# Kernel tuning notes

Measured on AMD Instinct MI355X. Metric: run time of the kernel, lower is better.

The kernel has to match this reference:

```python
import jax, jax.numpy as jnp
import numpy as np

B, N, DIM, H, DH = 4, 1024, 512, 8, 64
INNER = H * DH
LN_EPS = 1e-5


def layernorm(x, g, b):
    m = x.mean(-1, keepdims=True)
    v = jnp.var(x, axis=-1, keepdims=True)
    return (x - m) / jnp.sqrt(v + LN_EPS) * g + b


def setup_inputs() -> dict:
    key = jax.random.key(0)
    ks = jax.random.split(key, 8)
    return {
        "q": jax.random.normal(ks[0], (B, N, DIM), jnp.float32),
        "k": jax.random.normal(ks[1], (B, N, DIM), jnp.float32),
        "v": jax.random.normal(ks[2], (B, N, DIM), jnp.float32),
        "ln_g": jnp.ones((DIM,), jnp.float32),
        "ln_b": jnp.zeros((DIM,), jnp.float32),
        "W_in": jax.random.normal(ks[3], (INNER, DIM), jnp.float32) * 0.02,
        "W_out": jax.random.normal(ks[4], (DIM, INNER), jnp.float32) * 0.02,
        "b_out": jnp.zeros((DIM,), jnp.float32),
        "wp_W1": jax.random.normal(ks[5], (DH, 2 * DH), jnp.float32) * 0.05,
        "wp_b1": jnp.zeros((DH,), jnp.float32),
        "wp_ln_g": jnp.ones((DH,), jnp.float32),
        "wp_ln_b": jnp.zeros((DH,), jnp.float32),
        "wp_W2": jax.random.normal(ks[6], (3, DH), jnp.float32) * 0.05,
        "wp_b2": jnp.zeros((3,), jnp.float32),
    }


def reference(q, k, v, ln_g, ln_b, W_in, W_out, b_out,
              wp_W1, wp_b1, wp_ln_g, wp_ln_b, wp_W2, wp_b2):
    b, n, _ = q.shape

    def proj(t):  # [b, n, dim] -> [h, b, n, d]
        y = layernorm(t, ln_g, ln_b) @ W_in.T
        return y.reshape(b, n, H, DH).transpose(2, 0, 1, 3)

    f_q, f_k, f_v = proj(q), proj(k), proj(v)

    # cosine similarity component: [h, b, n, m]
    dots = jnp.einsum('hbnd,hbmd->hbnm', f_q, f_k)
    qn = jnp.linalg.norm(f_q, axis=-1)  # [h, b, n]
    kn = jnp.linalg.norm(f_k, axis=-1)  # [h, b, m]
    cosine_sim = dots / (qn[..., :, None] * kn[..., None, :])

    # centered covariance component
    q_c = f_q - f_q.mean(-1, keepdims=True)
    k_c = f_k - f_k.mean(-1, keepdims=True)
    cov_component = jnp.einsum('hbnd,hbmd->hbnm', q_c, k_c) / DH

    # variance-product component (outer product of per-row variances, unbiased like torch.var)
    q_var = jnp.var(f_q, axis=-1, ddof=1)  # [h, b, n]
    k_var = jnp.var(f_k, axis=-1, ddof=1)  # [h, b, m]
    var_component = (q_var[..., :, None] * k_var[..., None, :]) / DH

    # dynamic per-head mixing weights
    q_global = f_q.mean(axis=(1, 2))  # [h, d]
    k_global = f_k.mean(axis=(1, 2))  # [h, d]
    feats = jnp.concatenate([q_global, k_global], axis=-1)  # [h, 2d]
    hdn = jax.nn.relu(layernorm(feats @ wp_W1.T + wp_b1, wp_ln_g, wp_ln_b))
    weights = jax.nn.softmax(hdn @ wp_W2.T + wp_b2, axis=-1)  # [h, 3]
    w = weights[:, :, None, None, None]  # [h, 3, 1, 1, 1]

    mixed = w[:, 0] * cosine_sim + w[:, 1] * cov_component + w[:, 2] * var_component
    out = jnp.einsum('hbnm,hbmd->hbnd', mixed, f_v)
    out = out.transpose(1, 2, 0, 3).reshape(b, n, INNER)  # 'h b n d -> b n (h d)'
    return out @ W_out.T + b_out
```

## Files before the change

### kernel.cpp

```cpp
#include <hip/hip_runtime.h>
#include <hip/hip_bf16.h>

#define LN_EPS 1e-5f
typedef __attribute__((ext_vector_type(8))) short short8v;
typedef __attribute__((ext_vector_type(4))) short short4v;
typedef __attribute__((ext_vector_type(4))) float f32x4;
typedef __hip_bfloat16 bf16;

__device__ inline float wred_sum(float v) {
#pragma unroll
  for (int off = 1; off < 64; off <<= 1) v += __shfl_xor(v, off, 64);
  return v;
}
__device__ inline float b2f(short s) {
  return __uint_as_float(((unsigned)(unsigned short)s) << 16);
}
__device__ inline short f2bs(float x) {
  union { bf16 h; short s; } u; u.h = __float2bfloat16(x); return u.s;
}
__device__ inline float rbf(float x) {
  return __bfloat162float(__float2bfloat16(x));
}

__global__ __launch_bounds__(256) void lncvt_kernel(
    const float* __restrict__ q, const float* __restrict__ k,
    const float* __restrict__ v,
    const float* __restrict__ g, const float* __restrict__ bln,
    const float* __restrict__ Wi, const float* __restrict__ Wo,
    bf16* __restrict__ abf, bf16* __restrict__ Wib, bf16* __restrict__ Wob) {
  int bid = blockIdx.x, tid = threadIdx.x;
  if (bid < 3072) {
    int wave = tid >> 6, lane = tid & 63;
    int grow = bid * 4 + wave;
    int tensor = grow >> 12, row = grow & 4095;
    const float* src = tensor == 0 ? q : (tensor == 1 ? k : v);
    const float4* p = (const float4*)(src + (size_t)row * 512 + lane * 8);
    float4 a = p[0], b = p[1];
    float s  = a.x + a.y + a.z + a.w + b.x + b.y + b.z + b.w;
    float ss = a.x*a.x + a.y*a.y + a.z*a.z + a.w*a.w
             + b.x*b.x + b.y*b.y + b.z*b.z + b.w*b.w;
    s = wred_sum(s);
    ss = wred_sum(ss);
    float m = s * (1.f / 512.f);
    float r = rsqrtf(ss * (1.f / 512.f) - m * m + LN_EPS);
    float4 g0 = *(const float4*)(g + lane * 8);
    float4 g1 = *(const float4*)(g + lane * 8 + 4);
    float4 b0 = *(const float4*)(bln + lane * 8);
    float4 b1 = *(const float4*)(bln + lane * 8 + 4);
    short8v t;
    t[0] = f2bs((a.x - m) * r * g0.x + b0.x);
    t[1] = f2bs((a.y - m) * r * g0.y + b0.y);
    t[2] = f2bs((a.z - m) * r * g0.z + b0.z);
    t[3] = f2bs((a.w - m) * r * g0.w + b0.w);
    t[4] = f2bs((b.x - m) * r * g1.x + b1.x);
    t[5] = f2bs((b.y - m) * r * g1.y + b1.y);
    t[6] = f2bs((b.z - m) * r * g1.z + b1.z);
    t[7] = f2bs((b.w - m) * r * g1.w + b1.w);
    *(short8v*)(abf + (size_t)grow * 512 + lane * 8) = t;
  } else {
    int e0 = ((bid - 3072) * 256 + tid) * 8;
    float4 a = *(const float4*)(Wi + e0);
    float4 b = *(const float4*)(Wi + e0 + 4);
    short8v t;
    t[0] = f2bs(a.x); t[1] = f2bs(a.y); t[2] = f2bs(a.z); t[3] = f2bs(a.w);
    t[4] = f2bs(b.x); t[5] = f2bs(b.y); t[6] = f2bs(b.z); t[7] = f2bs(b.w);
    *(short8v*)(Wib + e0) = t;
    a = *(const float4*)(Wo + e0);
    b = *(const float4*)(Wo + e0 + 4);
    t[0] = f2bs(a.x); t[1] = f2bs(a.y); t[2] = f2bs(a.z); t[3] = f2bs(a.w);
    t[4] = f2bs(b.x); t[5] = f2bs(b.y); t[6] = f2bs(b.z); t[7] = f2bs(b.w);
    *(short8v*)(Wob + e0) = t;
  }
}

__global__ __launch_bounds__(256) void proj_kernel(
    const bf16* __restrict__ Asrc, const bf16* __restrict__ Wb,
    bf16* __restrict__ f_q, bf16* __restrict__ fkt, bf16* __restrict__ fkh,
    bf16* __restrict__ fvt,
    float* __restrict__ rn, float* __restrict__ mn, float* __restrict__ vr,
    float* __restrict__ gp) {
  __shared__ __attribute__((aligned(16))) bf16 As[64 * 64];
  __shared__ __attribute__((aligned(16))) bf16 Bs[128 * 64];
  __shared__ float gpbuf[4][128];
  int tid = threadIdx.x;
  int bj = blockIdx.x, bi = blockIdx.y;
  int row0 = bi * 64;
  int wv = tid >> 6, l = tid & 63, fr = l & 15, lq = l >> 4;
  f32x4 acc[8];
#pragma unroll
  for (int j = 0; j < 8; ++j)
#pragma unroll
    for (int e = 0; e < 4; ++e) acc[j][e] = 0.f;

  int swz = (fr & 7) << 4;

  for (int ks = 0; ks < 512; ks += 64) {
#pragma unroll
    for (int c = 0; c < 2; ++c) {
      int off = wv * 2048 + c * 1024 + l * 16;
      int ar = off >> 7;
      int sc = (off & 127) ^ ((ar & 7) << 4);
      const char* gsrc = (const char*)(Asrc + (size_t)(row0 + ar) * 512 + ks) + sc;
      __builtin_amdgcn_global_load_lds(gsrc, (char*)As + wv * 2048 + c * 1024, 16, 0, 0);
    }
#pragma unroll
    for (int c = 0; c < 4; ++c) {
      int off = wv * 4096 + c * 1024 + l * 16;
      int br = off >> 7;
      int sc = (off & 127) ^ ((br & 7) << 4);
      const char* gsrc = (const char*)(Wb + (size_t)(bj * 128 + br) * 512 + ks) + sc;
      __builtin_amdgcn_global_load_lds(gsrc, (char*)Bs + wv * 4096 + c * 1024, 16, 0, 0);
    }
    __syncthreads();
#pragma unroll
    for (int kk = 0; kk < 64; kk += 32) {
      int csw = (kk * 2 + lq * 16) ^ swz;
      short8v af = *(const short8v*)&As[(wv * 16 + fr) * 64 + (csw >> 1)];
#pragma unroll
      for (int j = 0; j < 8; ++j) {
        short8v bv = *(const short8v*)&Bs[(j * 16 + fr) * 64 + (csw >> 1)];
        acc[j] = __builtin_amdgcn_mfma_f32_16x16x32_bf16(af, bv, acc[j], 0, 0, 0);
      }
    }
    __syncthreads();
  }

  int tensor = bi >> 6, rb = bi & 63;
  int b = rb >> 4, n0 = (rb & 15) * 64;
  int nbase = n0 + wv * 16 + lq * 4;
  if (tensor == 2) {
#pragma unroll
    for (int j = 0; j < 8; ++j) {
      int h = bj * 2 + (j >> 2), hb = h * 4 + b;
      int dv = (j & 3) * 16 + fr;
      short4v t;
#pragma unroll
      for (int rr = 0; rr < 4; ++rr) t[rr] = f2bs(acc[j][rr]);
      *(short4v*)(fvt + (size_t)(hb * 64 + dv) * 1024 + nbase) = t;
    }
    return;
  }
  float vb[8][4];
#pragma unroll
  for (int j = 0; j < 8; ++j)
#pragma unroll
    for (int rr = 0; rr < 4; ++rr) vb[j][rr] = rbf(acc[j][rr]);

#pragma unroll
  for (int hh = 0; hh < 2; ++hh) {
    int h = bj * 2 + hh, hb = h * 4 + b;
    float sr[4], s2[4];
#pragma unroll
    for (int rr = 0; rr < 4; ++rr) {
      float s = 0.f, ss = 0.f;
#pragma unroll
      for (int jj = 0; jj < 4; ++jj) {
        float x = vb[hh * 4 + jj][rr];
        s += x; ss += x * x;
      }
#pragma unroll
      for (int off = 1; off < 16; off <<= 1) {
        s += __shfl_xor(s, off, 64);
        ss += __shfl_xor(ss, off, 64);
      }
      sr[rr] = s; s2[rr] = ss;
    }
    if (tensor == 0) {
#pragma unroll
      for (int jj = 0; jj < 4; ++jj) {
        int d = jj * 16 + fr;
#pragma unroll
        for (int rr = 0; rr < 4; ++rr)
          f_q[(size_t)(b * 1024 + nbase + rr) * 512 + h * 64 + d] =
              __float2bfloat16(acc[hh * 4 + jj][rr]);
      }
      if (fr == 0)
#pragma unroll
        for (int rr = 0; rr < 4; ++rr) {
          size_t idx = (size_t)hb * 1024 + nbase + rr;
          float mean = sr[rr] * (1.f / 64.f);
          rn[idx] = rsqrtf(s2[rr]);
          mn[idx] = mean;
          vr[idx] = (s2[rr] - 64.f * mean * mean) * (1.f / 63.f);
        }
    } else {
      float rnv[4];
#pragma unroll
      for (int rr = 0; rr < 4; ++rr) rnv[rr] = rsqrtf(s2[rr]);
#pragma unroll
      for (int jj = 0; jj < 4; ++jj) {
        int dk = jj * 16 + fr;
        short4v tp, th;
#pragma unroll
        for (int rr = 0; rr < 4; ++rr) {
          tp[rr] = f2bs(acc[hh * 4 + jj][rr]);
          th[rr] = f2bs(vb[hh * 4 + jj][rr] * rnv[rr]);
        }
        size_t off = (size_t)(hb * 64 + dk) * 1024 + nbase;
        *(short4v*)(fkt + off) = tp;
        *(short4v*)(fkh + off) = th;
      }
      if (fr == 0)
#pragma unroll
        for (int rr = 0; rr < 4; ++rr) {
          size_t idx = 32768 + (size_t)hb * 1024 + nbase + rr;
          float mean = sr[rr] * (1.f / 64.f);
          mn[idx] = mean;
          vr[idx] = (s2[rr] - 64.f * mean * mean) * (1.f / 63.f);
        }
    }
  }
#pragma unroll
  for (int j = 0; j < 8; ++j) {
    float c = 0.f;
#pragma unroll
    for (int rr = 0; rr < 4; ++rr) c += vb[j][rr];
    c += __shfl_xor(c, 16, 64);
    c += __shfl_xor(c, 32, 64);
    if (lq == 0) gpbuf[wv][j * 16 + fr] = c;
  }
  __syncthreads();
  if (tid < 128)
    gp[(size_t)(tensor * 64 + rb) * 512 + bj * 128 + tid] =
        gpbuf[0][tid] + gpbuf[1][tid] + gpbuf[2][tid] + gpbuf[3][tid];
}

__global__ __launch_bounds__(256) void outproj_kernel(
    const bf16* __restrict__ Ab, const bf16* __restrict__ Wb,
    const float* __restrict__ bias, float* __restrict__ out) {
  __shared__ __attribute__((aligned(16))) bf16 As[64 * 64];
  __shared__ __attribute__((aligned(16))) bf16 Bs[128 * 64];
  int tid = threadIdx.x;
  int bj = blockIdx.x, bi = blockIdx.y;
  int row0 = bi * 64;
  int wv = tid >> 6, l = tid & 63, fr = l & 15, lq = l >> 4;
  f32x4 acc[8];
#pragma unroll
  for (int j = 0; j < 8; ++j)
#pragma unroll
    for (int e = 0; e < 4; ++e) acc[j][e] = 0.f;

  int swz = (fr & 7) << 4;

  for (int ks = 0; ks < 512; ks += 64) {
#pragma unroll
    for (int c = 0; c < 2; ++c) {
      int off = wv * 2048 + c * 1024 + l * 16;
      int ar = off >> 7;
      int sc = (off & 127) ^ ((ar & 7) << 4);
      const char* gsrc = (const char*)(Ab + (size_t)(row0 + ar) * 512 + ks) + sc;
      __builtin_amdgcn_global_load_lds(gsrc, (char*)As + wv * 2048 + c * 1024, 16, 0, 0);
    }
#pragma unroll
    for (int c = 0; c < 4; ++c) {
      int off = wv * 4096 + c * 1024 + l * 16;
      int br = off >> 7;
      int sc = (off & 127) ^ ((br & 7) << 4);
      const char* gsrc = (const char*)(Wb + (size_t)(bj * 128 + br) * 512 + ks) + sc;
      __builtin_amdgcn_global_load_lds(gsrc, (char*)Bs + wv * 4096 + c * 1024, 16, 0, 0);
    }
    __syncthreads();
#pragma unroll
    for (int kk = 0; kk < 64; kk += 32) {
      int csw = (kk * 2 + lq * 16) ^ swz;
      short8v af = *(const short8v*)&As[(wv * 16 + fr) * 64 + (csw >> 1)];
#pragma unroll
      for (int j = 0; j < 8; ++j) {
        short8v bv = *(const short8v*)&Bs[(j * 16 + fr) * 64 + (csw >> 1)];
        acc[j] = __builtin_amdgcn_mfma_f32_16x16x32_bf16(af, bv, acc[j], 0, 0, 0);
      }
    }
    __syncthreads();
  }
#pragma unroll
  for (int j = 0; j < 8; ++j) {
    int col = bj * 128 + j * 16 + fr;
    float bvv = bias[col];
#pragma unroll
    for (int rr = 0; rr < 4; ++rr)
      out[(size_t)(row0 + wv * 16 + lq * 4 + rr) * 512 + col] = acc[j][rr] + bvv;
  }
}

__global__ __launch_bounds__(256) void aux_kernel(
    const bf16* __restrict__ fvt, const bf16* __restrict__ fkt,
    const bf16* __restrict__ fkh,
    const float* __restrict__ mn, const float* __restrict__ vr,
    const float* __restrict__ gp,
    const float* __restrict__ W1, const float* __restrict__ b1,
    const float* __restrict__ lg, const float* __restrict__ lb,
    const float* __restrict__ W2, const float* __restrict__ b2,
    float* __restrict__ part, float* __restrict__ kvm, float* __restrict__ kvv,
    float* __restrict__ wts) {
  __shared__ float sh[2560];
  int bid = blockIdx.x, tid = threadIdx.x;
  int wv = tid >> 6, l = tid & 63, fr = l & 15, lq = l >> 4;
  if (bid < 128) {
    int hb = bid >> 2, mc = bid & 3;
    f32x4 apl[4], aht[4];
#pragma unroll
    for (int j = 0; j < 4; ++j)
#pragma unroll
      for (int e = 0; e < 4; ++e) { apl[j][e] = 0.f; aht[j][e] = 0.f; }
    size_t arow = (size_t)(hb * 64 + wv * 16 + fr) * 1024;
#pragma unroll 2
    for (int m0 = 0; m0 < 256; m0 += 32) {
      size_t moff = mc * 256 + m0 + lq * 8;
      short8v av = *(const short8v*)(fvt + arow + moff);
#pragma unroll
      for (int j = 0; j < 4; ++j) {
        size_t brow = (size_t)(hb * 64 + j * 16 + fr) * 1024 + moff;
        short8v bp = *(const short8v*)(fkt + brow);
        short8v bh = *(const short8v*)(fkh + brow);
        apl[j] = __builtin_amdgcn_mfma_f32_16x16x32_bf16(av, bp, apl[j], 0, 0, 0);
        aht[j] = __builtin_amdgcn_mfma_f32_16x16x32_bf16(av, bh, aht[j], 0, 0, 0);
      }
    }
    size_t base = (size_t)(hb * 4 + mc) * 8192;
#pragma unroll
    for (int j = 0; j < 4; ++j)
#pragma unroll
      for (int rr = 0; rr < 4; ++rr) {
        int dv = wv * 16 + lq * 4 + rr, dk = j * 16 + fr;
        part[base + dv * 64 + dk] = apl[j][rr];
        part[base + 4096 + dv * 64 + dk] = aht[j][rr];
      }
  } else if (bid < 160) {
    int hb = bid - 128;
    float* kmL = sh; float* kvL = sh + 1024; float* red = sh + 2048;
    for (int i = tid; i < 1024; i += 256) {
      kmL[i] = mn[32768 + hb * 1024 + i];
      kvL[i] = vr[32768 + hb * 1024 + i];
    }
    __syncthreads();
    int dv = tid >> 2, seg = tid & 3;
    float am = 0.f, av = 0.f;
    size_t rowb = (size_t)(hb * 64 + dv) * 1024 + seg * 256;
    for (int i = 0; i < 256; i += 8) {
      short8v vv = *(const short8v*)(fvt + rowb + i);
#pragma unroll
      for (int e = 0; e < 8; ++e) {
        float f = b2f(vv[e]);
        am += kmL[seg * 256 + i + e] * f;
        av += kvL[seg * 256 + i + e] * f;
      }
    }
    red[dv * 4 + seg] = am;
    red[256 + dv * 4 + seg] = av;
    __syncthreads();
    if (tid < 64) {
      kvm[hb * 64 + tid] = red[tid * 4] + red[tid * 4 + 1] + red[tid * 4 + 2] + red[tid * 4 + 3];
      kvv[hb * 64 + tid] = red[256 + tid * 4] + red[256 + tid * 4 + 1] +
                           red[256 + tid * 4 + 2] + red[256 + tid * 4 + 3];
    }
  } else {
    int h = bid - 160;
    float* red = sh;
    float* fqv = sh + 512;
    float* fkv = sh + 576;
    float* pred = sh + 640;
    int cl = tid & 63, part4 = tid >> 6;
    float sq = 0.f, sk = 0.f;
#pragma unroll
    for (int p = 0; p < 16; ++p) {
      sq += gp[(size_t)(part4 * 16 + p) * 512 + h * 64 + cl];
      sk += gp[(size_t)(64 + part4 * 16 + p) * 512 + h * 64 + cl];
    }
    red[part4 * 128 + cl] = sq;
    red[part4 * 128 + 64 + cl] = sk;
    __syncthreads();
    if (tid < 128) {
      float vsum = red[tid] + red[128 + tid] + red[256 + tid] + red[384 + tid];
      if (tid < 64) fqv[tid] = vsum * (1.f / 4096.f);
      else          fkv[tid - 64] = vsum * (1.f / 4096.f);
    }
    __syncthreads();
    int j = tid & 63;
    float pp = 0.f;
#pragma unroll
    for (int i = 0; i < 16; ++i) {
      pp += fqv[part4 * 16 + i] * W1[j * 128 + part4 * 16 + i];
      pp += fkv[part4 * 16 + i] * W1[j * 128 + 64 + part4 * 16 + i];
    }
    pred[part4 * 64 + j] = pp;
    __syncthreads();
    if (tid < 64) {
      float pre = b1[j] + pred[j] + pred[64 + j] + pred[128 + j] + pred[192 + j];
      float s = wred_sum(pre);
      float ss = wred_sum(pre * pre);
      float mean = s * (1.f / 64.f);
      float var = ss * (1.f / 64.f) - mean * mean;
      float hdn = (pre - mean) * rsqrtf(var + LN_EPS) * lg[j] + lb[j];
      hdn = fmaxf(hdn, 0.f);
      float l0 = wred_sum(hdn * W2[0 * 64 + j]) + b2[0];
      float l1 = wred_sum(hdn * W2[1 * 64 + j]) + b2[1];
      float l2 = wred_sum(hdn * W2[2 * 64 + j]) + b2[2];
      float mx = fmaxf(l0, fmaxf(l1, l2));
      float e0 = __expf(l0 - mx), e1 = __expf(l1 - mx), e2 = __expf(l2 - mx);
      float inv = 1.f / (e0 + e1 + e2);
      if (j == 0) {
        wts[h * 3 + 0] = e0 * inv;
        wts[h * 3 + 1] = e1 * inv;
        wts[h * 3 + 2] = e2 * inv;
      }
    }
  }
}

__global__ __launch_bounds__(256) void apply_kernel(
    const bf16* __restrict__ f_q, const float* __restrict__ Gpart,
    const float* __restrict__ rn, const float* __restrict__ mn,
    const float* __restrict__ vr, const float* __restrict__ wts,
    const float* __restrict__ kvm, const float* __restrict__ kvv,
    bf16* __restrict__ attnb) {
  __shared__ bf16 Qs[64 * 72];
  __shared__ bf16 Ap[64 * 72];
  __shared__ bf16 Ah[64 * 72];
  __shared__ float qrnL[64], qmnL[64], qvrL[64], kvmL[64], kvvL[64];
  int qt = blockIdx.x, hbid = blockIdx.y;
  int h = hbid >> 2, b = hbid & 3;
  int tid = threadIdx.x;
  int wv = tid >> 6, l = tid & 63, fr = l & 15, lq = l >> 4;
  {
    int row = tid >> 2, qq = (tid & 3) * 16;
    const bf16* qsrc = f_q + (size_t)(b * 1024 + qt * 64 + row) * 512 + h * 64 + qq;
    *(short8v*)&Qs[row * 72 + qq] = *(const short8v*)qsrc;
    *(short8v*)&Qs[row * 72 + qq + 8] = *(const short8v*)(qsrc + 8);
    const float* psrc = Gpart + (size_t)hbid * 32768 + row * 64 + qq;
#pragma unroll
    for (int c = 0; c < 4; ++c) {
      float4 spl = {0.f, 0.f, 0.f, 0.f}, sht = {0.f, 0.f, 0.f, 0.f};
#pragma unroll
      for (int mc = 0; mc < 4; ++mc) {
        float4 p = *(const float4*)(psrc + mc * 8192 + c * 4);
        float4 t = *(const float4*)(psrc + mc * 8192 + 4096 + c * 4);
        spl.x += p.x; spl.y += p.y; spl.z += p.z; spl.w += p.w;
        sht.x += t.x; sht.y += t.y; sht.z += t.z; sht.w += t.w;
      }
      Ap[row * 72 + qq + c * 4 + 0] = __float2bfloat16(spl.x);
      Ap[row * 72 + qq + c * 4 + 1] = __float2bfloat16(spl.y);
      Ap[row * 72 + qq + c * 4 + 2] = __float2bfloat16(spl.z);
      Ap[row * 72 + qq + c * 4 + 3] = __float2bfloat16(spl.w);
      Ah[row * 72 + qq + c * 4 + 0] = __float2bfloat16(sht.x);
      Ah[row * 72 + qq + c * 4 + 1] = __float2bfloat16(sht.y);
      Ah[row * 72 + qq + c * 4 + 2] = __float2bfloat16(sht.z);
      Ah[row * 72 + qq + c * 4 + 3] = __float2bfloat16(sht.w);
    }
  }
  if (tid < 64) {
    qrnL[tid] = rn[(size_t)hbid * 1024 + qt * 64 + tid];
    qmnL[tid] = mn[(size_t)hbid * 1024 + qt * 64 + tid];
    qvrL[tid] = vr[(size_t)hbid * 1024 + qt * 64 + tid];
    kvmL[tid] = kvm[hbid * 64 + tid];
    kvvL[tid] = kvv[hbid * 64 + tid];
  }
  __syncthreads();
  f32x4 ap_[4], ah_[4];
#pragma unroll
  for (int j = 0; j < 4; ++j)
#pragma unroll
    for (int e = 0; e < 4; ++e) { ap_[j][e] = 0.f; ah_[j][e] = 0.f; }
#pragma unroll
  for (int kk = 0; kk < 64; kk += 32) {
    short8v aq = *(const short8v*)&Qs[(wv * 16 + fr) * 72 + kk + lq * 8];
#pragma unroll
    for (int j = 0; j < 4; ++j) {
      short8v bp = *(const short8v*)&Ap[(j * 16 + fr) * 72 + kk + lq * 8];
      short8v bh = *(const short8v*)&Ah[(j * 16 + fr) * 72 + kk + lq * 8];
      ap_[j] = __builtin_amdgcn_mfma_f32_16x16x32_bf16(aq, bp, ap_[j], 0, 0, 0);
      ah_[j] = __builtin_amdgcn_mfma_f32_16x16x32_bf16(aq, bh, ah_[j], 0, 0, 0);
    }
  }
  float w0 = wts[h * 3 + 0], w1 = wts[h * 3 + 1], w2 = wts[h * 3 + 2];
  float f1 = w1 * (1.f / 64.f), w264 = w2 * (1.f / 64.f);
#pragma unroll
  for (int j = 0; j < 4; ++j) {
    int dv = j * 16 + fr;
    float km = kvmL[dv], kv2 = kvvL[dv];
#pragma unroll
    for (int rr = 0; rr < 4; ++rr) {
      int n = wv * 16 + lq * 4 + rr;
      float o = w0 * qrnL[n] * ah_[j][rr] + f1 * ap_[j][rr]
              - w1 * qmnL[n] * km + w264 * qvrL[n] * kv2;
      attnb[(size_t)(b * 1024 + qt * 64 + n) * 512 + h * 64 + dv] = __float2bfloat16(o);
    }
  }
}

extern "C" void kernel_launch(void* const* d_in, const int* in_sizes, int n_in,
                              void* d_out, int out_size, void* d_ws, size_t ws_size,
                              hipStream_t stream) {
  const float* q     = (const float*)d_in[0];
  const float* k     = (const float*)d_in[1];
  const float* v     = (const float*)d_in[2];
  const float* ln_g  = (const float*)d_in[3];
  const float* ln_b  = (const float*)d_in[4];
  const float* W_in  = (const float*)d_in[5];
  const float* W_out = (const float*)d_in[6];
  const float* b_out = (const float*)d_in[7];
  const float* wp_W1 = (const float*)d_in[8];
  const float* wp_b1 = (const float*)d_in[9];
  const float* wp_lg = (const float*)d_in[10];
  const float* wp_lb = (const float*)d_in[11];
  const float* wp_W2 = (const float*)d_in[12];
  const float* wp_b2 = (const float*)d_in[13];
  float* out = (float*)d_out;

  char* w8 = (char*)d_ws;
  bf16* abf   = (bf16*)(w8);
  float* Gpart = (float*)(w8);
  bf16* f_q   = (bf16*)(w8 + (12u << 20));
  bf16* fkt   = (bf16*)(w8 + (16u << 20));
  bf16* fkh   = (bf16*)(w8 + (20u << 20));
  bf16* fvt   = (bf16*)(w8 + (24u << 20));
  bf16* attnb = (bf16*)(w8 + (28u << 20));
  bf16* Wib   = (bf16*)(w8 + (32u << 20));
  bf16* Wob   = (bf16*)(w8 + (32u << 20) + (512u << 10));
  float* fb   = (float*)(w8 + (33u << 20));
  float* rn  = fb;
  float* mn  = fb + 32768;
  float* vr  = fb + 98304;
  float* gp  = fb + 163840;
  float* kvm = fb + 229376;
  float* kvv = fb + 231424;
  float* wts = fb + 233472;

  lncvt_kernel<<<3200, 256, 0, stream>>>(q, k, v, ln_g, ln_b, W_in, W_out,
                                         abf, Wib, Wob);
  proj_kernel<<<dim3(4, 192), 256, 0, stream>>>(
      abf, Wib, f_q, fkt, fkh, fvt, rn, mn, vr, gp);
  aux_kernel<<<168, 256, 0, stream>>>(
      fvt, fkt, fkh, mn, vr, gp, wp_W1, wp_b1, wp_lg, wp_lb, wp_W2, wp_b2,
      Gpart, kvm, kvv, wts);
  apply_kernel<<<dim3(16, 32), 256, 0, stream>>>(
      f_q, Gpart, rn, mn, vr, wts, kvm, kvv, attnb);
  outproj_kernel<<<dim3(4, 64), 256, 0, stream>>>(attnb, Wob, b_out, out);
}
```

Baseline: 63.82 us.

## Double-buffer LDS tiles in projection GEMMs with async global_load_lds prefetch

Projection and output-projection GEMM kernels now keep two LDS buffers for A and B tiles. While MFMAs run on the current k-slice, the next slice is issued with global_load_lds. Explicit vmcnt waits and raw s_barrier calls replace __syncthreads. This hides global-memory latency behind compute at the cost of doubling LDS use per block, which may reduce occupancy, and relies on hand-counted vmcnt correctness.

```diff
diff --git a/kernel.cpp b/kernel.cpp
--- a/kernel.cpp
+++ b/kernel.cpp
@@ -79,8 +79,8 @@
     bf16* __restrict__ fvt,
     float* __restrict__ rn, float* __restrict__ mn, float* __restrict__ vr,
     float* __restrict__ gp) {
-  __shared__ __attribute__((aligned(16))) bf16 As[64 * 64];
-  __shared__ __attribute__((aligned(16))) bf16 Bs[128 * 64];
+  __shared__ __attribute__((aligned(16))) bf16 As[2][64 * 64];
+  __shared__ __attribute__((aligned(16))) bf16 Bs[2][128 * 64];
   __shared__ float gpbuf[4][128];
   int tid = threadIdx.x;
   int bj = blockIdx.x, bi = blockIdx.y;
@@ -93,37 +93,53 @@
     for (int e = 0; e < 4; ++e) acc[j][e] = 0.f;
 
   int swz = (fr & 7) << 4;
-
-  for (int ks = 0; ks < 512; ks += 64) {
-#pragma unroll
-    for (int c = 0; c < 2; ++c) {
-      int off = wv * 2048 + c * 1024 + l * 16;
-      int ar = off >> 7;
-      int sc = (off & 127) ^ ((ar & 7) << 4);
-      const char* gsrc = (const char*)(Asrc + (size_t)(row0 + ar) * 512 + ks) + sc;
-      __builtin_amdgcn_global_load_lds(gsrc, (char*)As + wv * 2048 + c * 1024, 16, 0, 0);
-    }
-#pragma unroll
-    for (int c = 0; c < 4; ++c) {
-      int off = wv * 4096 + c * 1024 + l * 16;
-      int br = off >> 7;
-      int sc = (off & 127) ^ ((br & 7) << 4);
-      const char* gsrc = (const char*)(Wb + (size_t)(bj * 128 + br) * 512 + ks) + sc;
-      __builtin_amdgcn_global_load_lds(gsrc, (char*)Bs + wv * 4096 + c * 1024, 16, 0, 0);
-    }
-    __syncthreads();
+  int offA0 = wv * 2048 + l * 16;
+  int offB0 = wv * 4096 + l * 16;
+
+#define STAGE(buf, ks)                                                        \
+  {                                                                           \
+    _Pragma("unroll")                                                         \
+    for (int c = 0; c < 2; ++c) {                                             \
+      int off = offA0 + c * 1024;                                             \
+      int ar = off >> 7;                                                      \
+      int sc = (off & 127) ^ ((ar & 7) << 4);                                 \
+      const char* gsrc = (const char*)(Asrc + (size_t)(row0 + ar) * 512 + (ks)) + sc; \
+      __builtin_amdgcn_global_load_lds(gsrc, (char*)As[buf] + wv * 2048 + c * 1024, 16, 0, 0); \
+    }                                                                         \
+    _Pragma("unroll")                                                         \
+    for (int c = 0; c < 4; ++c) {                                             \
+      int off = offB0 + c * 1024;                                             \
+      int br = off >> 7;                                                      \
+      int sc = (off & 127) ^ ((br & 7) << 4);                                 \
+      const char* gsrc = (const char*)(Wb + (size_t)(bj * 128 + br) * 512 + (ks)) + sc; \
+      __builtin_amdgcn_global_load_lds(gsrc, (char*)Bs[buf] + wv * 4096 + c * 1024, 16, 0, 0); \
+    }                                                                         \
+  }
+
+  STAGE(0, 0);
+#pragma unroll
+  for (int t = 0; t < 8; ++t) {
+    int cur = t & 1;
+    if (t < 7) {
+      STAGE(cur ^ 1, (t + 1) * 64);
+      asm volatile("s_waitcnt vmcnt(6)" ::: "memory");
+    } else {
+      asm volatile("s_waitcnt vmcnt(0)" ::: "memory");
+    }
+    __builtin_amdgcn_s_barrier();
 #pragma unroll
     for (int kk = 0; kk < 64; kk += 32) {
       int csw = (kk * 2 + lq * 16) ^ swz;
-      short8v af = *(const short8v*)&As[(wv * 16 + fr) * 64 + (csw >> 1)];
+      short8v af = *(const short8v*)&As[cur][(wv * 16 + fr) * 64 + (csw >> 1)];
 #pragma unroll
       for (int j = 0; j < 8; ++j) {
-        short8v bv = *(const short8v*)&Bs[(j * 16 + fr) * 64 + (csw >> 1)];
+        short8v bv = *(const short8v*)&Bs[cur][(j * 16 + fr) * 64 + (csw >> 1)];
         acc[j] = __builtin_amdgcn_mfma_f32_16x16x32_bf16(af, bv, acc[j], 0, 0, 0);
       }
     }
-    __syncthreads();
-  }
+    __builtin_amdgcn_s_barrier();
+  }
+#undef STAGE
 
   int tensor = bi >> 6, rb = bi & 63;
   int b = rb >> 4, n0 = (rb & 15) * 64;
@@ -228,8 +244,8 @@
 __global__ __launch_bounds__(256) void outproj_kernel(
     const bf16* __restrict__ Ab, const bf16* __restrict__ Wb,
     const float* __restrict__ bias, float* __restrict__ out) {
-  __shared__ __attribute__((aligned(16))) bf16 As[64 * 64];
-  __shared__ __attribute__((aligned(16))) bf16 Bs[128 * 64];
+  __shared__ __attribute__((aligned(16))) bf16 As[2][64 * 64];
+  __shared__ __attribute__((aligned(16))) bf16 Bs[2][128 * 64];
   int tid = threadIdx.x;
   int bj = blockIdx.x, bi = blockIdx.y;
   int row0 = bi * 64;
@@ -241,37 +257,53 @@
     for (int e = 0; e < 4; ++e) acc[j][e] = 0.f;
 
   int swz = (fr & 7) << 4;
-
-  for (int ks = 0; ks < 512; ks += 64) {
-#pragma unroll
-    for (int c = 0; c < 2; ++c) {
-      int off = wv * 2048 + c * 1024 + l * 16;
-      int ar = off >> 7;
-      int sc = (off & 127) ^ ((ar & 7) << 4);
-      const char* gsrc = (const char*)(Ab + (size_t)(row0 + ar) * 512 + ks) + sc;
-      __builtin_amdgcn_global_load_lds(gsrc, (char*)As + wv * 2048 + c * 1024, 16, 0, 0);
-    }
-#pragma unroll
-    for (int c = 0; c < 4; ++c) {
-      int off = wv * 4096 + c * 1024 + l * 16;
-      int br = off >> 7;
-      int sc = (off & 127) ^ ((br & 7) << 4);
-      const char* gsrc = (const char*)(Wb + (size_t)(bj * 128 + br) * 512 + ks) + sc;
-      __builtin_amdgcn_global_load_lds(gsrc, (char*)Bs + wv * 4096 + c * 1024, 16, 0, 0);
-    }
-    __syncthreads();
+  int offA0 = wv * 2048 + l * 16;
+  int offB0 = wv * 4096 + l * 16;
+
+#define STAGE(buf, ks)                                                        \
+  {                                                                           \
+    _Pragma("unroll")                                                         \
+    for (int c = 0; c < 2; ++c) {                                             \
+      int off = offA0 + c * 1024;                                             \
+      int ar = off >> 7;                                                      \
+      int sc = (off & 127) ^ ((ar & 7) << 4);                                 \
+      const char* gsrc = (const char*)(Ab + (size_t)(row0 + ar) * 512 + (ks)) + sc; \
+      __builtin_amdgcn_global_load_lds(gsrc, (char*)As[buf] + wv * 2048 + c * 1024, 16, 0, 0); \
+    }                                                                         \
+    _Pragma("unroll")                                                         \
+    for (int c = 0; c < 4; ++c) {                                             \
+      int off = offB0 + c * 1024;                                             \
+      int br = off >> 7;                                                      \
+      int sc = (off & 127) ^ ((br & 7) << 4);                                 \
+      const char* gsrc = (const char*)(Wb + (size_t)(bj * 128 + br) * 512 + (ks)) + sc; \
+      __builtin_amdgcn_global_load_lds(gsrc, (char*)Bs[buf] + wv * 4096 + c * 1024, 16, 0, 0); \
+    }                                                                         \
+  }
+
+  STAGE(0, 0);
+#pragma unroll
+  for (int t = 0; t < 8; ++t) {
+    int cur = t & 1;
+    if (t < 7) {
+      STAGE(cur ^ 1, (t + 1) * 64);
+      asm volatile("s_waitcnt vmcnt(6)" ::: "memory");
+    } else {
+      asm volatile("s_waitcnt vmcnt(0)" ::: "memory");
+    }
+    __builtin_amdgcn_s_barrier();
 #pragma unroll
     for (int kk = 0; kk < 64; kk += 32) {
       int csw = (kk * 2 + lq * 16) ^ swz;
-      short8v af = *(const short8v*)&As[(wv * 16 + fr) * 64 + (csw >> 1)];
+      short8v af = *(const short8v*)&As[cur][(wv * 16 + fr) * 64 + (csw >> 1)];
 #pragma unroll
       for (int j = 0; j < 8; ++j) {
-        short8v bv = *(const short8v*)&Bs[(j * 16 + fr) * 64 + (csw >> 1)];
+        short8v bv = *(const short8v*)&Bs[cur][(j * 16 + fr) * 64 + (csw >> 1)];
         acc[j] = __builtin_amdgcn_mfma_f32_16x16x32_bf16(af, bv, acc[j], 0, 0, 0);
       }
     }
-    __syncthreads();
-  }
+    __builtin_amdgcn_s_barrier();
+  }
+#undef STAGE
 #pragma unroll
   for (int j = 0; j < 8; ++j) {
     int col = bj * 128 + j * 16 + fr;
```

Measured after the change: 63.78 us. No clear change (-0.1%).
